# Optimization experiments

Measured on AMD Instinct MI355X. Metric: run time of the kernel, lower is better.

The kernel has to match this reference:

```python
import jax, jax.numpy as jnp
import numpy as np

# Module constants (from init_kwargs)
BETA = 0.1
DX = 10.0 / 2048  # X / N
DT = 0.002        # CFL: 0.75 * dx / max|f'|
BATCH = 128
N = 2048
STEPNUM = 256


def flux(u):
    # f_real with is_real=True:
    # f = 0.5*u*(3 - u^2) + beta/12 * u^2 * (3/4 - 2u + 3/2 u^2 - 1/4 u^4)
    u2 = u * u
    return 0.5 * u * (3.0 - u2) + (BETA / 12.0) * u2 * (
        0.75 - 2.0 * u + 1.5 * u2 - 0.25 * u2 * u2)


def flux_prime(u):
    # Closed-form elementwise derivative of flux (what torch autograd.grad computes
    # per grid point, since f is elementwise in u):
    # f'(u) = 1.5*(1 - u^2) + beta/12 * (1.5u - 6u^2 + 6u^3 - 1.5u^5)
    u2 = u * u
    u3 = u2 * u
    return 1.5 * (1.0 - u2) + (BETA / 12.0) * (
        1.5 * u - 6.0 * u2 + 6.0 * u3 - 1.5 * u2 * u3)


def setup_inputs() -> dict:
    key = jax.random.key(0)
    init = jax.random.uniform(key, (BATCH, N), dtype=jnp.float32)  # u in [0,1]
    return {"init": init, "stepnum": STEPNUM}


def reference(init, stepnum):
    dt_over_dx = jnp.float32(DT / DX)

    def step(u, _):
        f = flux(u)                              # [B, N]
        a = jnp.abs(flux_prime(u))               # [B, N]
        # Local Lax-Friedrichs (Rusanov) wave speed: max over the 2-point stencil
        alpha = jnp.maximum(a[:, :-1], a[:, 1:])  # [B, N-1]
        f_half = 0.5 * (f[:, :-1] + f[:, 1:]) - 0.5 * alpha * (u[:, 1:] - u[:, :-1])
        # Interior update for j = 1..N-2
        u_inner = u[:, 1:-1] - dt_over_dx * (f_half[:, 1:] - f_half[:, :-1])
        # Outflow boundaries: u[0] = u[1], u[N-1] = u[N-2] (with u[1], u[N-2] updated)
        u_new = jnp.concatenate([u_inner[:, :1], u_inner, u_inner[:, -1:]], axis=1)
        return u_new, u_new

    _, traj = jax.lax.scan(step, init, None, length=stepnum - 1)  # [S-1, B, N]
    return jnp.concatenate([init[None], traj], axis=0)           # [S, B, N]
```

## Files before the change

kernel.cpp:

```cpp
#include <hip/hip_runtime.h>

#define BATCH 128
#define NCELL 2048

constexpr float BETA = 0.1f;
constexpr double DT = 0.002;
constexpr double DX = 10.0 / 2048.0;

__device__ __forceinline__ float flux(float u) {
    float u2 = u * u;
    return 0.5f * u * (3.0f - u2) +
           (BETA / 12.0f) * u2 * (0.75f - 2.0f * u + 1.5f * u2 - 0.25f * u2 * u2);
}

__device__ __forceinline__ float flux_prime_abs(float u) {
    float u2 = u * u;
    float u3 = u2 * u;
    float fp = 1.5f * (1.0f - u2) +
               (BETA / 12.0f) * (1.5f * u - 6.0f * u2 + 6.0f * u3 - 1.5f * u2 * u3);
    return fabsf(fp);
}

__global__ __launch_bounds__(1024)
void VariantCoeLinear1d_kernel(const float* __restrict__ init,
                               const int* __restrict__ stepnum_p,
                               float* __restrict__ out) {
    __shared__ float uA[NCELL];
    __shared__ float uB[NCELL];
    __shared__ float fs[NCELL];
    __shared__ float as_[NCELL];

    const int b = blockIdx.x;
    const int t = threadIdx.x;
    const int S = *stepnum_p;
    const float c = (float)(DT / DX);

    const float* row_in = init + (size_t)b * NCELL;

    float u0 = row_in[t];
    float u1 = row_in[t + 1024];
    uA[t] = u0;
    uA[t + 1024] = u1;
    out[(size_t)b * NCELL + t] = u0;
    out[(size_t)b * NCELL + t + 1024] = u1;

    float* ucur = uA;
    float* unxt = uB;

    for (int s = 1; s < S; ++s) {
        __syncthreads();
        {
            float uc0 = ucur[t];
            float uc1 = ucur[t + 1024];
            fs[t] = flux(uc0);
            as_[t] = flux_prime_abs(uc0);
            fs[t + 1024] = flux(uc1);
            as_[t + 1024] = flux_prime_abs(uc1);
        }
        __syncthreads();
        float* __restrict__ orow = out + (size_t)s * (BATCH * NCELL) + (size_t)b * NCELL;
#pragma unroll
        for (int k = 0; k < 2; ++k) {
            const int j = t + k * 1024;
            int jj = j;
            if (j == 0) jj = 1;
            if (j == NCELL - 1) jj = NCELL - 2;
            const float um = ucur[jj - 1], uz = ucur[jj], up = ucur[jj + 1];
            const float fm = fs[jj - 1],  fz = fs[jj],  fp = fs[jj + 1];
            const float am = as_[jj - 1], az = as_[jj], ap = as_[jj + 1];
            const float fh_r = 0.5f * (fz + fp) - 0.5f * fmaxf(az, ap) * (up - uz);
            const float fh_l = 0.5f * (fm + fz) - 0.5f * fmaxf(am, az) * (uz - um);
            const float un = uz - c * (fh_r - fh_l);
            unxt[j] = un;
            orow[j] = un;
        }
        float* tmp = ucur;
        ucur = unxt;
        unxt = tmp;
    }
}

extern "C" void kernel_launch(void* const* d_in, const int* in_sizes, int n_in,
                              void* d_out, int out_size, void* d_ws, size_t ws_size,
                              hipStream_t stream) {
    const float* init = (const float*)d_in[0];
    const int* stepnum = (const int*)d_in[1];
    float* out = (float*)d_out;

    dim3 grid(BATCH);
    dim3 block(1024);
    VariantCoeLinear1d_kernel<<<grid, block, 0, stream>>>(init, stepnum, out);
}
```

Measured before the change: 384.6 us.

## Split each row across two blocks with halo overlap and register-resident stencil

```diff
diff --git a/kernel.cpp b/kernel.cpp
--- a/kernel.cpp
+++ b/kernel.cpp
@@ -2,81 +2,105 @@
 
 #define BATCH 128
 #define NCELL 2048
+#define HALO 256
+#define WIDTH 1536
+#define NTHREADS 384
 
-constexpr float BETA = 0.1f;
-constexpr double DT = 0.002;
-constexpr double DX = 10.0 / 2048.0;
-
-__device__ __forceinline__ float flux(float u) {
-    float u2 = u * u;
-    return 0.5f * u * (3.0f - u2) +
-           (BETA / 12.0f) * u2 * (0.75f - 2.0f * u + 1.5f * u2 - 0.25f * u2 * u2);
+__device__ __forceinline__ float flux_h(float u, float u2) {
+    float h = fmaf(u2, -0.0020833333333333333f, 0.0125f);
+    h = fmaf(u, h, -0.5166666666666667f);
+    h = fmaf(u, h, 0.00625f);
+    h = fmaf(u, h, 1.5f);
+    return u * h;
+}
+__device__ __forceinline__ float aprime_h(float u, float u2) {
+    float h = fmaf(u2, -0.0125f, 0.05f);
+    h = fmaf(u, h, -1.55f);
+    h = fmaf(u, h, 0.0125f);
+    h = fmaf(u, h, 1.5f);
+    return fabsf(h);
 }
 
-__device__ __forceinline__ float flux_prime_abs(float u) {
-    float u2 = u * u;
-    float u3 = u2 * u;
-    float fp = 1.5f * (1.0f - u2) +
-               (BETA / 12.0f) * (1.5f * u - 6.0f * u2 + 6.0f * u3 - 1.5f * u2 * u3);
-    return fabsf(fp);
-}
-
-__global__ __launch_bounds__(1024)
+__global__ __launch_bounds__(NTHREADS)
 void VariantCoeLinear1d_kernel(const float* __restrict__ init,
                                const int* __restrict__ stepnum_p,
                                float* __restrict__ out) {
-    __shared__ float uA[NCELL];
-    __shared__ float uB[NCELL];
-    __shared__ float fs[NCELL];
-    __shared__ float as_[NCELL];
+    __shared__ float ubuf[2][WIDTH];
 
     const int b = blockIdx.x;
+    const int row = b >> 1;
+    const int half = b & 1;
     const int t = threadIdx.x;
     const int S = *stepnum_p;
-    const float c = (float)(DT / DX);
+    const float c = 0.4096f;
 
-    const float* row_in = init + (size_t)b * NCELL;
+    const int ownedLo = half << 10;
+    const int ownedHi = ownedLo + 1023;
+    const int base = ownedLo - HALO;
+    const int li = t << 2;
+    const int g0 = base + li;
 
-    float u0 = row_in[t];
-    float u1 = row_in[t + 1024];
-    uA[t] = u0;
-    uA[t + 1024] = u1;
-    out[(size_t)b * NCELL + t] = u0;
-    out[(size_t)b * NCELL + t + 1024] = u1;
+    const float* rin = init + (size_t)row * NCELL;
+    float u0, u1, u2, u3;
+    if (g0 >= 0 && g0 + 3 < NCELL) {
+        float4 v = *(const float4*)(rin + g0);
+        u0 = v.x; u1 = v.y; u2 = v.z; u3 = v.w;
+    } else {
+        u0 = rin[min(max(g0 + 0, 0), NCELL - 1)];
+        u1 = rin[min(max(g0 + 1, 0), NCELL - 1)];
+        u2 = rin[min(max(g0 + 2, 0), NCELL - 1)];
+        u3 = rin[min(max(g0 + 3, 0), NCELL - 1)];
+    }
 
-    float* ucur = uA;
-    float* unxt = uB;
+    const bool owned = (t >= HALO / 4) && (t < (HALO + 1024) / 4);
+    if (owned) {
+        *(float4*)(out + (size_t)row * NCELL + g0) = make_float4(u0, u1, u2, u3);
+    }
 
+    int cur = 0;
     for (int s = 1; s < S; ++s) {
+        float* ub = ubuf[cur];
+        *(float4*)&ub[li] = make_float4(u0, u1, u2, u3);
         __syncthreads();
-        {
-            float uc0 = ucur[t];
-            float uc1 = ucur[t + 1024];
-            fs[t] = flux(uc0);
-            as_[t] = flux_prime_abs(uc0);
-            fs[t + 1024] = flux(uc1);
-            as_[t + 1024] = flux_prime_abs(uc1);
+
+        const int rem = (S - 1) - s;
+        const int lo = max(ownedLo - rem, 0);
+        const int hi = min(ownedHi + rem, NCELL - 1);
+
+        if (g0 + 3 >= lo && g0 <= hi) {
+            const float ulm = ub[max(li - 1, 0)];
+            const float ulp = ub[min(li + 4, WIDTH - 1)];
+            float ul[6] = {ulm, u0, u1, u2, u3, ulp};
+            float f[6], a[6];
+#pragma unroll
+            for (int j = 0; j < 6; ++j) {
+                const float uu = ul[j], uu2 = uu * uu;
+                f[j] = flux_h(uu, uu2);
+                a[j] = aprime_h(uu, uu2);
+            }
+            float fh[5];
+#pragma unroll
+            for (int j = 0; j < 5; ++j) {
+                fh[j] = 0.5f * (f[j] + f[j + 1])
+                      - 0.5f * fmaxf(a[j], a[j + 1]) * (ul[j + 1] - ul[j]);
+            }
+            float un[4];
+#pragma unroll
+            for (int i = 0; i < 4; ++i) {
+                un[i] = ul[i + 1] - c * (fh[i + 1] - fh[i]);
+                const int g = g0 + i;
+                un[i] = (g >= lo && g <= hi) ? un[i] : ul[i + 1];
+            }
+            if (g0 == 0) un[0] = un[1];
+            if (g0 + 3 == NCELL - 1) un[3] = un[2];
+            u0 = un[0]; u1 = un[1]; u2 = un[2]; u3 = un[3];
+
+            if (owned) {
+                *(float4*)(out + ((size_t)s * BATCH + row) * NCELL + g0) =
+                    make_float4(u0, u1, u2, u3);
+            }
         }
-        __syncthreads();
-        float* __restrict__ orow = out + (size_t)s * (BATCH * NCELL) + (size_t)b * NCELL;
-#pragma unroll
-        for (int k = 0; k < 2; ++k) {
-            const int j = t + k * 1024;
-            int jj = j;
-            if (j == 0) jj = 1;
-            if (j == NCELL - 1) jj = NCELL - 2;
-            const float um = ucur[jj - 1], uz = ucur[jj], up = ucur[jj + 1];
-            const float fm = fs[jj - 1],  fz = fs[jj],  fp = fs[jj + 1];
-            const float am = as_[jj - 1], az = as_[jj], ap = as_[jj + 1];
-            const float fh_r = 0.5f * (fz + fp) - 0.5f * fmaxf(az, ap) * (up - uz);
-            const float fh_l = 0.5f * (fm + fz) - 0.5f * fmaxf(am, az) * (uz - um);
-            const float un = uz - c * (fh_r - fh_l);
-            unxt[j] = un;
-            orow[j] = un;
-        }
-        float* tmp = ucur;
-        ucur = unxt;
-        unxt = tmp;
+        cur ^= 1;
     }
 }
 
@@ -87,7 +111,7 @@
     const int* stepnum = (const int*)d_in[1];
     float* out = (float*)d_out;
 
-    dim3 grid(BATCH);
-    dim3 block(1024);
+    dim3 grid(BATCH * 2);
+    dim3 block(NTHREADS);
     VariantCoeLinear1d_kernel<<<grid, block, 0, stream>>>(init, stepnum, out);
 }
```

Measured after the change: 342.1 us. -11.0%, faster.
